# Kernel optimization log

Measured on AMD Instinct MI355X. Metric: run time of the kernel, lower is better.

The kernel has to match this reference:

```python
import jax, jax.numpy as jnp
import numpy as np

B, N, F_IN, H = 16, 1024, 64, 256
NEG = -9e15
ALPHA = 0.2  # LeakyReLU slope


def _leaky(x):
    return jnp.where(x >= 0, x, ALPHA * x)


def setup_inputs() -> dict:
    key = jax.random.key(0)
    ks = jax.random.split(key, 12)
    s = lambda k, shape, fan: jax.random.normal(k, shape, jnp.float32) / np.sqrt(fan)
    node_features = jax.random.normal(ks[0], (B, N, F_IN), jnp.float32)
    adj_matrix = jax.random.randint(ks[1], (B, N, N), 0, 2).astype(jnp.float32)
    return {
        "node_features": node_features,
        "adj_matrix": adj_matrix,
        "emb_W": s(ks[2], (F_IN, H), F_IN),
        "emb_b": jnp.zeros((H,), jnp.float32),
        "W0": s(ks[3], (H, H), H),
        "a1_0": s(ks[4], (H,), H),
        "a2_0": s(ks[5], (H,), H),
        "W1": s(ks[6], (H, H), H),
        "a1_1": s(ks[7], (H,), H),
        "a2_1": s(ks[8], (H,), H),
        "gp_W1": s(ks[9], (H, H), H),
        "gp_b1": jnp.zeros((H,), jnp.float32),
        "gp_W2": s(ks[10], (H, H), H),
        "gp_b2": jnp.zeros((H,), jnp.float32),
    }


def _gat_layer(x, mask, W, a1, a2):
    # x: [B,N,H]; mask: [B,N,N] bool. Equivalent to original concat trick:
    # a([h_i || h_j]) = h_i @ a1 + h_j @ a2 with a.weight split in halves.
    h = jnp.einsum('bnf,fo->bno', x, W)              # [B,N,H]
    s1 = jnp.einsum('bnh,h->bn', h, a1)              # [B,N]
    s2 = jnp.einsum('bnh,h->bn', h, a2)              # [B,N]
    e = _leaky(s1[:, :, None] + s2[:, None, :])      # [B,N,N]
    att = jax.nn.softmax(jnp.where(mask, e, NEG), axis=2)
    # dropout p=0.2 is identity in eval mode
    return jnp.einsum('bij,bjh->bih', att, h)        # [B,N,H]


def reference(node_features, adj_matrix, emb_W, emb_b,
              W0, a1_0, a2_0, W1, a1_1, a2_1,
              gp_W1, gp_b1, gp_W2, gp_b2):
    mask = adj_matrix > 0
    x = jnp.einsum('bnf,fh->bnh', node_features, emb_W) + emb_b
    x = jax.nn.relu(_gat_layer(x, mask, W0, a1_0, a2_0))
    x = jax.nn.relu(_gat_layer(x, mask, W1, a1_1, a2_1))
    g = jnp.mean(x, axis=1) + jnp.max(x, axis=1)     # [B,H]
    g = jax.nn.relu(g @ gp_W1 + gp_b1) @ gp_W2 + gp_b2
    return x, g
```

## Files before the change

### kernel.cpp

```cpp
#include <hip/hip_runtime.h>
#include <hip/hip_bf16.h>

#define B 16
#define N 1024
#define F_IN 64
#define H 256
#define ALPHA 0.2f
#define LOG2E 1.44269504f

typedef __attribute__((ext_vector_type(8))) _Float16 half8;
typedef __attribute__((ext_vector_type(4))) _Float16 half4;
typedef __attribute__((ext_vector_type(4))) float floatx4;
typedef __attribute__((ext_vector_type(16))) float floatx16;

#if __has_builtin(__builtin_amdgcn_exp2f)
#define EXP2F(x) __builtin_amdgcn_exp2f(x)
#else
#define EXP2F(x) exp2f(x)
#endif

__device__ __forceinline__ floatx4 mfma_f16(half8 a, half8 b, floatx4 c) {
    return __builtin_amdgcn_mfma_f32_16x16x32_f16(a, b, c, 0, 0, 0);
}
__device__ __forceinline__ floatx16 mfma32_f16(half8 a, half8 b, floatx16 c) {
    return __builtin_amdgcn_mfma_f32_32x32x16_f16(a, b, c, 0, 0, 0);
}

__global__ __launch_bounds__(256) void k_front(const float* __restrict__ adj,
                                               const float* __restrict__ embW,
                                               const float* __restrict__ W0, const float* __restrict__ W1,
                                               const float* __restrict__ a10, const float* __restrict__ a20,
                                               const float* __restrict__ a11, const float* __restrict__ a21,
                                               unsigned* __restrict__ mask32,
                                               _Float16* __restrict__ wBf,
                                               _Float16* __restrict__ embf,
                                               float* __restrict__ wa1, float* __restrict__ wa2) {
    __shared__ float lds[256 * 17];
    const int blk = blockIdx.x;
    const int t = threadIdx.x;
    const int lane = t & 63;

    if (blk < 1024) {
        const int wv = blk * 4 + (t >> 6);
#pragma unroll 2
        for (int task = wv; task < B * N * 4; task += 4096) {
            const float4 v = *(const float4*)(adj + (size_t)task * 256 + lane * 4);
            unsigned long long b0 = __ballot(v.x > 0.f);
            unsigned long long b1 = __ballot(v.y > 0.f);
            unsigned long long b2 = __ballot(v.z > 0.f);
            unsigned long long b3 = __ballot(v.w > 0.f);
            if (lane < 8) {
                unsigned w0 = (unsigned)((b0 >> (8 * lane)) & 0xff)
                            | ((unsigned)((b1 >> (8 * lane)) & 0xff) << 8)
                            | ((unsigned)((b2 >> (8 * lane)) & 0xff) << 16)
                            | ((unsigned)((b3 >> (8 * lane)) & 0xff) << 24);
                const int jg = task & 3, row = task >> 2;
                mask32[(size_t)row * 32 + jg * 8 + lane] = w0;
            }
        }
        return;
    }
    const int pb = blk - 1024;
    if (pb == 34) {
        for (int s = t; s < 2048; s += 256) {
            const int ln = s & 63, ct2 = s >> 6;
            const int ct = ct2 >> 1, ks2 = ct2 & 1;
            const int q = ln >> 4, lw = ln & 15;
            half8 bf;
#pragma unroll
            for (int e = 0; e < 8; e++)
                bf[e] = (_Float16)embW[(ks2 * 32 + q * 8 + e) * H + ct * 16 + lw];
            *(half8*)(embf + (size_t)s * 8) = bf;
        }
        return;
    }
    if (pb >= 32) {
        const int l = pb - 32;
        const float* W = l ? W1 : W0;
        const float* a1 = l ? a11 : a10;
        const float* a2 = l ? a21 : a20;
        float* a1s = lds;
        float* a2s = lds + 256;
        a1s[t] = a1[t]; a2s[t] = a2[t];
        __syncthreads();
        float v1 = 0.f, v2 = 0.f;
        for (int c = 0; c < H; c += 4) {
            float4 w = *(const float4*)&W[t * H + c];
            v1 += w.x * a1s[c] + w.y * a1s[c + 1] + w.z * a1s[c + 2] + w.w * a1s[c + 3];
            v2 += w.x * a2s[c] + w.y * a2s[c + 1] + w.z * a2s[c + 2] + w.w * a2s[c + 3];
        }
        wa1[l * H + t] = v1;
        wa2[l * H + t] = v2;
        return;
    }
    const int l = pb >> 4, ct = pb & 15;
    const float* W = l ? W1 : W0;
#pragma unroll
    for (int rep = 0; rep < 16; rep++) {
        int idx = rep * 256 + t;
        int k = idx >> 4, cl = idx & 15;
        lds[k * 17 + cl] = W[k * H + ct * 16 + cl];
    }
    __syncthreads();
    const int w = t >> 6;
    const int l15 = lane & 15, quad = lane >> 4;
#pragma unroll
    for (int e = 0; e < 2; e++) {
        const int ks = w * 2 + e;
        half8 bf;
#pragma unroll
        for (int jj = 0; jj < 8; jj++)
            bf[jj] = (_Float16)lds[(ks * 32 + quad * 8 + jj) * 17 + l15];
        *(half8*)(wBf + (size_t)(((l * 16 + ct) * 8 + ks) * 64 + lane) * 8) = bf;
    }
}

#define XS(it, ks) ((((it) * 8 + (ks))) * 520)
template <int EMB>
__global__ __launch_bounds__(256, 4) void k_gemm(const _Float16* __restrict__ xf,
                                                 const float* __restrict__ nf,
                                                 const _Float16* __restrict__ embf,
                                                 const float* __restrict__ embB,
                                                 const _Float16* __restrict__ wBf,
                                                 const float* __restrict__ wa1, const float* __restrict__ wa2,
                                                 _Float16* __restrict__ hB,
                                                 float* __restrict__ s1, float* __restrict__ s2) {
    __shared__ __align__(16) _Float16 sm[8320];
    const int lin = blockIdx.x;
    const int rc = lin >> 1, chalf = lin & 1;
    const int row0 = rc * 32;
    const int t = threadIdx.x;
    const int lane = t & 63, w = t >> 6;
    const int l15 = lane & 15, quad = lane >> 4;

    if (EMB) {
        half8 anf[2][2];
#pragma unroll
        for (int it = 0; it < 2; it++)
#pragma unroll
            for (int ks2 = 0; ks2 < 2; ks2++) {
                const float* src = nf + (size_t)(row0 + it * 16 + l15) * F_IN + ks2 * 32 + quad * 8;
                float4 f0 = *(const float4*)(src);
                float4 f1 = *(const float4*)(src + 4);
                half8 a;
                a[0] = (_Float16)f0.x; a[1] = (_Float16)f0.y;
                a[2] = (_Float16)f0.z; a[3] = (_Float16)f0.w;
                a[4] = (_Float16)f1.x; a[5] = (_Float16)f1.y;
                a[6] = (_Float16)f1.z; a[7] = (_Float16)f1.w;
                anf[it][ks2] = a;
            }
#pragma unroll
        for (int ctl = 0; ctl < 4; ctl++) {
            const int ct = w * 4 + ctl;
            half8 be0 = *(const half8*)(embf + (size_t)((ct * 2 + 0) * 64 + lane) * 8);
            half8 be1 = *(const half8*)(embf + (size_t)((ct * 2 + 1) * 64 + lane) * 8);
            const int col = ct * 16 + l15;
            const float bias = embB[col];
            const int ks = col >> 5, qd = (col >> 3) & 3, e = col & 7;
#pragma unroll
            for (int it = 0; it < 2; it++) {
                floatx4 xa = {0.f, 0.f, 0.f, 0.f};
                xa = mfma_f16(anf[it][0], be0, xa);
                xa = mfma_f16(anf[it][1], be1, xa);
#pragma unroll
                for (int r = 0; r < 4; r++)
                    sm[XS(it, ks) + (qd * 16 + quad * 4 + r) * 8 + e] = (_Float16)(xa[r] + bias);
            }
        }
    } else {
#pragma unroll
        for (int pass = 0; pass < 4; pass++) {
            int idx = pass * 256 + t;
            int row_l = idx >> 5, k8 = idx & 31;
            half8 v = *(const half8*)(xf + (size_t)(row0 + row_l) * H + k8 * 8);
            int it = row_l >> 4, lf = row_l & 15, ks = k8 >> 2, qd = k8 & 3;
            *(half8*)(sm + XS(it, ks) + (qd * 16 + lf) * 8) = v;
        }
    }
    __syncthreads();

    const int ct0 = chalf * 8 + 2 * w;
    const _Float16* pB0 = wBf + (size_t)((ct0 * 8) * 64 + lane) * 8;
    const _Float16* pB1 = wBf + (size_t)(((ct0 + 1) * 8) * 64 + lane) * 8;

    floatx4 acc[2][2];
    floatx4 z = {0.f, 0.f, 0.f, 0.f};
    acc[0][0] = z; acc[0][1] = z; acc[1][0] = z; acc[1][1] = z;
    float sp1a = 0.f, sp2a = 0.f, sp1b = 0.f, sp2b = 0.f;

    half8 B0 = *(const half8*)(pB0);
    half8 B1 = *(const half8*)(pB1);

#pragma unroll
    for (int ks = 0; ks < 8; ks++) {
        half8 nB0 = B0, nB1 = B1;
        if (ks < 7) {
            const int o = (ks + 1) * 512;
            nB0 = *(const half8*)(pB0 + o);
            nB1 = *(const half8*)(pB1 + o);
        }
        half8 A0 = *(const half8*)(sm + XS(0, ks) + lane * 8);
        half8 A1 = *(const half8*)(sm + XS(1, ks) + lane * 8);
        acc[0][0] = mfma_f16(A0, B0, acc[0][0]);
        acc[0][1] = mfma_f16(A0, B1, acc[0][1]);
        acc[1][0] = mfma_f16(A1, B0, acc[1][0]);
        acc[1][1] = mfma_f16(A1, B1, acc[1][1]);
        if (chalf == 0 && w == 0) {
            float4 w1a = *(const float4*)(wa1 + ks * 32 + quad * 8);
            float4 w1b = *(const float4*)(wa1 + ks * 32 + quad * 8 + 4);
            float4 w2a = *(const float4*)(wa2 + ks * 32 + quad * 8);
            float4 w2b = *(const float4*)(wa2 + ks * 32 + quad * 8 + 4);
            float wv1[8] = {w1a.x, w1a.y, w1a.z, w1a.w, w1b.x, w1b.y, w1b.z, w1b.w};
            float wv2[8] = {w2a.x, w2a.y, w2a.z, w2a.w, w2b.x, w2b.y, w2b.z, w2b.w};
#pragma unroll
            for (int j = 0; j < 8; j++) {
                float xa = (float)A0[j];
                float xb = (float)A1[j];
                sp1a += xa * wv1[j]; sp2a += xa * wv2[j];
                sp1b += xb * wv1[j]; sp2b += xb * wv2[j];
            }
        }
        B0 = nB0; B1 = nB1;
    }

    __syncthreads();
    _Float16* trc = sm;
#pragma unroll
    for (int rg = 0; rg < 2; rg++) {
#pragma unroll
        for (int n2 = 0; n2 < 2; n2++) {
            const int c_l = (2 * w + n2) * 16 + l15;
            half4 hv;
            hv[0] = (_Float16)acc[rg][n2][0];
            hv[1] = (_Float16)acc[rg][n2][1];
            hv[2] = (_Float16)acc[rg][n2][2];
            hv[3] = (_Float16)acc[rg][n2][3];
            *(half4*)(trc + c_l * 40 + rg * 16 + quad * 4) = hv;
        }
    }
    __syncthreads();
    {
        const int bb = row0 >> 10, jtb = (row0 >> 5) & 31;
#pragma unroll
        for (int rep = 0; rep < 2; rep++) {
            int slot = rep * 256 + t;
            int l = slot & 63, frag = slot >> 6;
            int k4 = frag >> 1, ks = frag & 1;
            int c_l = k4 * 32 + (l & 31);
            int roff = ks * 16 + (l >> 5) * 8;
            half8 hv = *(const half8*)(trc + c_l * 40 + roff);
            _Float16* dst = hB + ((size_t)((bb * 8 + chalf * 4 + k4) * 32 + jtb) * 2 + ks) * 512 + l * 8;
            *(half8*)dst = hv;
        }
    }
    if (chalf == 0 && w == 0) {
        sp1a += __shfl_xor(sp1a, 16); sp1a += __shfl_xor(sp1a, 32);
        sp2a += __shfl_xor(sp2a, 16); sp2a += __shfl_xor(sp2a, 32);
        sp1b += __shfl_xor(sp1b, 16); sp1b += __shfl_xor(sp1b, 32);
        sp2b += __shfl_xor(sp2b, 16); sp2b += __shfl_xor(sp2b, 32);
        if (quad == 0) {
            s1[row0 + l15] = sp1a; s2[row0 + l15] = sp2a;
            s1[row0 + 16 + l15] = sp1b; s2[row0 + 16 + l15] = sp2b;
        }
    }
}

template <int LAST>
__global__ __launch_bounds__(256, 1) void k_gat(const _Float16* __restrict__ hB,
                                                const float* __restrict__ s1g,
                                                const float* __restrict__ s2g,
                                                const unsigned* __restrict__ mask32,
                                                float* __restrict__ outf,
                                                _Float16* __restrict__ oxf,
                                                float* __restrict__ psum, float* __restrict__ pmax) {
    __shared__ float s2s[N];
    __shared__ unsigned msk[128][33];
    __shared__ float wmax[4];
    __shared__ float red1[4][128];
    __shared__ float red2[4][128];
    const int lin = blockIdx.x;
    const int xcd = lin & 7, sl = lin >> 3;
    const int b = xcd * 2 + (sl & 1);
    const int chunk = (sl >> 1) & 7;
    const int chalf = sl >> 4;
    const int i0 = chunk * 128;
    const int t = threadIdx.x;
    const int lane = t & 63, w = t >> 6;
    const int l31 = lane & 31, hi = lane >> 5;
    const int hi2 = hi * 2, hi8 = hi * 8;

    float tm = -INFINITY;
    for (int idx = t; idx < N; idx += 256) {
        float v = s2g[b * N + idx] * LOG2E;
        s2s[idx] = v;
        tm = fmaxf(tm, v);
    }
#pragma unroll
    for (int off = 1; off <= 32; off <<= 1) tm = fmaxf(tm, __shfl_xor(tm, off));
    if (lane == 0) wmax[w] = tm;
#pragma unroll
    for (int pass = 0; pass < 16; pass++) {
        int idx = pass * 256 + t;
        int r = idx >> 5, wd = idx & 31;
        msk[r][wd] = mask32[(size_t)(b * N + i0 + r) * 32 + wd];
    }
    __syncthreads();
    const float s2maxL = fmaxf(fmaxf(wmax[0], wmax[1]), fmaxf(wmax[2], wmax[3]));

    const float s1L = s1g[b * N + i0 + w * 32 + l31] * LOG2E;
    const float tmx = s1L + s2maxL;
    const float mL = fmaxf(tmx, ALPHA * tmx);
    const float a1c = s1L - mL;
    const float a2c = fmaf(ALPHA, s1L, -mL);

    const _Float16* pb[4][2];
#pragma unroll
    for (int k4 = 0; k4 < 4; k4++)
#pragma unroll
        for (int ks = 0; ks < 2; ks++)
            pb[k4][ks] = hB + ((size_t)(b * 8 + chalf * 4 + k4) * 64 + ks) * 512 + lane * 8;

    floatx16 acc[4];
    floatx16 accl;
#pragma unroll
    for (int r = 0; r < 16; r++) accl[r] = 0.f;
#pragma unroll
    for (int k4 = 0; k4 < 4; k4++) acc[k4] = accl;

    half8 ones;
#pragma unroll
    for (int jj = 0; jj < 8; jj++) ones[jj] = (_Float16)1.0f;

    const float* svp = s2s + hi8;
    const unsigned* mr = &msk[w * 32 + l31][0];

    half8 bufA[4][2], bufB[4][2];
#pragma unroll
    for (int k4 = 0; k4 < 4; k4++) {
        bufA[k4][0] = *(const half8*)(pb[k4][0]);
        bufA[k4][1] = *(const half8*)(pb[k4][1]);
    }

#define GAT_STEP(JT, BUF)                                                      \
    do {                                                                       \
        const unsigned m = mr[JT];                                             \
        float4 sa0 = *(const float4*)(svp + (JT) * 32);                        \
        float4 sb0 = *(const float4*)(svp + (JT) * 32 + 4);                    \
        float4 sa1 = *(const float4*)(svp + (JT) * 32 + 16);                   \
        float4 sb1 = *(const float4*)(svp + (JT) * 32 + 20);                   \
        float sv0[8] = {sa0.x, sa0.y, sa0.z, sa0.w, sb0.x, sb0.y, sb0.z, sb0.w};\
        float sv1[8] = {sa1.x, sa1.y, sa1.z, sa1.w, sb1.x, sb1.y, sb1.z, sb1.w};\
        unsigned mq0 = m >> hi2;                                               \
        unsigned mq1 = m >> (4 + hi2);                                         \
        union { _Float16 h[8]; half8 v; } pk0, pk1;                            \
        _Pragma("unroll")                                                      \
        for (int e = 0; e < 8; e++) {                                          \
            const int bp = (e & 3) * 8 + (e >> 2);                             \
            float u0 = a1c + sv0[e];                                           \
            float v0 = fmaf(ALPHA, sv0[e], a2c);                               \
            float w0 = fmaxf(u0, v0);                                          \
            w0 = ((mq0 >> bp) & 1u) ? w0 : -126.f;                             \
            pk0.h[e] = (_Float16)EXP2F(w0);                                    \
            float u1 = a1c + sv1[e];                                           \
            float v1 = fmaf(ALPHA, sv1[e], a2c);                               \
            float w1 = fmaxf(u1, v1);                                          \
            w1 = ((mq1 >> bp) & 1u) ? w1 : -126.f;                             \
            pk1.h[e] = (_Float16)EXP2F(w1);                                    \
        }                                                                      \
        accl = mfma32_f16(pk0.v, ones, accl);                                  \
        _Pragma("unroll")                                                      \
        for (int k4 = 0; k4 < 4; k4++) acc[k4] = mfma32_f16(pk0.v, BUF[k4][0], acc[k4]); \
        accl = mfma32_f16(pk1.v, ones, accl);                                  \
        _Pragma("unroll")                                                      \
        for (int k4 = 0; k4 < 4; k4++) acc[k4] = mfma32_f16(pk1.v, BUF[k4][1], acc[k4]); \
    } while (0)

    for (int jt = 0; jt < 32; jt += 2) {
        {
            const int o = (jt + 1) * 1024;
#pragma unroll
            for (int k4 = 0; k4 < 4; k4++) {
                bufB[k4][0] = *(const half8*)(pb[k4][0] + o);
                bufB[k4][1] = *(const half8*)(pb[k4][1] + o);
            }
        }
        GAT_STEP(jt, bufA);
        if (jt + 2 < 32) {
            const int o = (jt + 2) * 1024;
#pragma unroll
            for (int k4 = 0; k4 < 4; k4++) {
                bufA[k4][0] = *(const half8*)(pb[k4][0] + o);
                bufA[k4][1] = *(const half8*)(pb[k4][1] + o);
            }
        }
        GAT_STEP(jt + 1, bufB);
    }
#undef GAT_STEP

    float invv[16];
#pragma unroll
    for (int r = 0; r < 16; r++) invv[r] = 1.f / accl[r];

    const size_t rowb = (size_t)b * N + i0 + w * 32 + 4 * hi;
    const int colbase = chalf * 128;
#pragma unroll
    for (int k4 = 0; k4 < 4; k4++) {
        const int c = colbase + k4 * 32 + l31;
        float cs = 0.f, cm = -INFINITY;
#pragma unroll
        for (int reg = 0; reg < 16; reg++) {
            const int roff = (reg & 3) + 8 * (reg >> 2);
            float v = fmaxf(acc[k4][reg] * invv[reg], 0.f);
            if (LAST) {
                outf[(rowb + roff) * H + c] = v;
                cs += v; cm = fmaxf(cm, v);
            } else {
                oxf[(rowb + roff) * H + c] = (_Float16)v;
            }
        }
        if (LAST) {
            cs += __shfl_xor(cs, 32);
            cm = fmaxf(cm, __shfl_xor(cm, 32));
            if (hi == 0) { red1[w][k4 * 32 + l31] = cs; red2[w][k4 * 32 + l31] = cm; }
        }
    }
    if (LAST) {
        __syncthreads();
        if (t < 128) {
            float s = red1[0][t] + red1[1][t] + red1[2][t] + red1[3][t];
            float m = fmaxf(fmaxf(red2[0][t], red2[1][t]), fmaxf(red2[2][t], red2[3][t]));
            psum[(b * 8 + chunk) * H + chalf * 128 + t] = s;
            pmax[(b * 8 + chunk) * H + chalf * 128 + t] = m;
        }
    }
}

__global__ __launch_bounds__(256) void k_pool2(const float* __restrict__ psum,
                                               const float* __restrict__ pmax,
                                               const float* __restrict__ W1, const float* __restrict__ b1,
                                               const float* __restrict__ W2, const float* __restrict__ b2,
                                               float* __restrict__ gout) {
    __shared__ float g_s[H];
    __shared__ float t_s[H];
    const int b = blockIdx.x;
    const int c = threadIdx.x;
    float s = 0.f, m = -INFINITY;
#pragma unroll
    for (int ch = 0; ch < 8; ch++) {
        s += psum[(b * 8 + ch) * H + c];
        m = fmaxf(m, pmax[(b * 8 + ch) * H + c]);
    }
    g_s[c] = s * (1.f / N) + m;
    __syncthreads();
    float a = b1[c];
#pragma unroll 16
    for (int k = 0; k < H; k++) a += g_s[k] * W1[k * H + c];
    t_s[c] = fmaxf(a, 0.f);
    __syncthreads();
    float o = b2[c];
#pragma unroll 16
    for (int k = 0; k < H; k++) o += t_s[k] * W2[k * H + c];
    gout[b * H + c] = o;
}

extern "C" void kernel_launch(void* const* d_in, const int* in_sizes, int n_in,
                              void* d_out, int out_size, void* d_ws, size_t ws_size,
                              hipStream_t stream) {
    const float* nf    = (const float*)d_in[0];
    const float* adj   = (const float*)d_in[1];
    const float* emb_W = (const float*)d_in[2];
    const float* emb_b = (const float*)d_in[3];
    const float* W0    = (const float*)d_in[4];
    const float* a1_0  = (const float*)d_in[5];
    const float* a2_0  = (const float*)d_in[6];
    const float* W1    = (const float*)d_in[7];
    const float* a1_1  = (const float*)d_in[8];
    const float* a2_1  = (const float*)d_in[9];
    const float* gpW1  = (const float*)d_in[10];
    const float* gpb1  = (const float*)d_in[11];
    const float* gpW2  = (const float*)d_in[12];
    const float* gpb2  = (const float*)d_in[13];

    float* xout = (float*)d_out;
    float* gout = xout + B * N * H;

    char* w = (char*)d_ws;
    _Float16* xf     = (_Float16*)(w);
    _Float16* hB     = (_Float16*)(w + 8388608);
    unsigned* mask32 = (unsigned*)(w + 16777216);
    float* s1        = (float*)(w + 18874368);
    float* s2        = (float*)(w + 18939904);
    _Float16* wBf    = (_Float16*)(w + 19005440);
    float* wa1       = (float*)(w + 19267584);
    float* wa2       = (float*)(w + 19269632);
    float* psum      = (float*)(w + 19271680);
    float* pmax      = (float*)(w + 19533824);
    _Float16* embf   = (_Float16*)(w + 19795968);

    k_front<<<1059, 256, 0, stream>>>(adj, emb_W, W0, W1,
                                      a1_0, a2_0, a1_1, a2_1,
                                      mask32, wBf, embf, wa1, wa2);

    k_gemm<1><<<1024, 256, 0, stream>>>(nullptr, nf, embf, emb_b,
                                        wBf, wa1, wa2, hB, s1, s2);
    k_gat<0><<<256, 256, 0, stream>>>(hB, s1, s2, mask32, nullptr, xf,
                                      nullptr, nullptr);

    k_gemm<0><<<1024, 256, 0, stream>>>(xf, nullptr, nullptr, nullptr,
                                        wBf + 65536, wa1 + H, wa2 + H, hB, s1, s2);
    k_gat<1><<<256, 256, 0, stream>>>(hB, s1, s2, mask32, xout, nullptr,
                                      psum, pmax);

    k_pool2<<<B, 256, 0, stream>>>(psum, pmax, gpW1, gpb1, gpW2, gpb2, gout);
}
```

Before: 219.0 us.

## Overlap adjacency bitmask packing with embedding GEMM and fuse pooling into last GAT

The small weight-prep work moves into its own tiny kernel. The adjacency-to-bitmask packing now shares one launch with the first embedding/projection GEMM through interleaved block roles, so the memory-bound mask pass overlaps with the compute-bound GEMM. The graph pooling MLP is folded into the last GAT kernel using a per-batch atomic counter, where the last block to finish does the readout, which removes a separate launch. This adds atomic and ordering complexity, and the counter must be reset each call, which the prep kernel does.

```diff
diff --git a/kernel.cpp b/kernel.cpp
--- a/kernel.cpp
+++ b/kernel.cpp
@@ -26,22 +26,92 @@
     return __builtin_amdgcn_mfma_f32_32x32x16_f16(a, b, c, 0, 0, 0);
 }
 
-__global__ __launch_bounds__(256) void k_front(const float* __restrict__ adj,
-                                               const float* __restrict__ embW,
-                                               const float* __restrict__ W0, const float* __restrict__ W1,
-                                               const float* __restrict__ a10, const float* __restrict__ a20,
-                                               const float* __restrict__ a11, const float* __restrict__ a21,
-                                               unsigned* __restrict__ mask32,
-                                               _Float16* __restrict__ wBf,
-                                               _Float16* __restrict__ embf,
-                                               float* __restrict__ wa1, float* __restrict__ wa2) {
+__global__ __launch_bounds__(256) void k_prep(const float* __restrict__ embW,
+                                              const float* __restrict__ W0, const float* __restrict__ W1,
+                                              const float* __restrict__ a10, const float* __restrict__ a20,
+                                              const float* __restrict__ a11, const float* __restrict__ a21,
+                                              _Float16* __restrict__ wBf,
+                                              _Float16* __restrict__ embf,
+                                              float* __restrict__ wa1, float* __restrict__ wa2,
+                                              int* __restrict__ cnt) {
     __shared__ float lds[256 * 17];
     const int blk = blockIdx.x;
     const int t = threadIdx.x;
     const int lane = t & 63;
 
-    if (blk < 1024) {
-        const int wv = blk * 4 + (t >> 6);
+    if (blk == 34) {
+        if (t < B) cnt[t] = 0;
+        for (int s = t; s < 2048; s += 256) {
+            const int ln = s & 63, ct2 = s >> 6;
+            const int ct = ct2 >> 1, ks2 = ct2 & 1;
+            const int q = ln >> 4, lw = ln & 15;
+            half8 bf;
+#pragma unroll
+            for (int e = 0; e < 8; e++)
+                bf[e] = (_Float16)embW[(ks2 * 32 + q * 8 + e) * H + ct * 16 + lw];
+            *(half8*)(embf + (size_t)s * 8) = bf;
+        }
+        return;
+    }
+    if (blk >= 32) {
+        const int l = blk - 32;
+        const float* W = l ? W1 : W0;
+        const float* a1 = l ? a11 : a10;
+        const float* a2 = l ? a21 : a20;
+        float* a1s = lds;
+        float* a2s = lds + 256;
+        a1s[t] = a1[t]; a2s[t] = a2[t];
+        __syncthreads();
+        float v1 = 0.f, v2 = 0.f;
+        for (int c = 0; c < H; c += 4) {
+            float4 w = *(const float4*)&W[t * H + c];
+            v1 += w.x * a1s[c] + w.y * a1s[c + 1] + w.z * a1s[c + 2] + w.w * a1s[c + 3];
+            v2 += w.x * a2s[c] + w.y * a2s[c + 1] + w.z * a2s[c + 2] + w.w * a2s[c + 3];
+        }
+        wa1[l * H + t] = v1;
+        wa2[l * H + t] = v2;
+        return;
+    }
+    const int l = blk >> 4, ct = blk & 15;
+    const float* W = l ? W1 : W0;
+#pragma unroll
+    for (int rep = 0; rep < 16; rep++) {
+        int idx = rep * 256 + t;
+        int k = idx >> 4, cl = idx & 15;
+        lds[k * 17 + cl] = W[k * H + ct * 16 + cl];
+    }
+    __syncthreads();
+    const int w = t >> 6;
+    const int l15 = lane & 15, quad = lane >> 4;
+#pragma unroll
+    for (int e = 0; e < 2; e++) {
+        const int ks = w * 2 + e;
+        half8 bf;
+#pragma unroll
+        for (int jj = 0; jj < 8; jj++)
+            bf[jj] = (_Float16)lds[(ks * 32 + quad * 8 + jj) * 17 + l15];
+        *(half8*)(wBf + (size_t)(((l * 16 + ct) * 8 + ks) * 64 + lane) * 8) = bf;
+    }
+}
+
+#define XS(it, ks) ((((it) * 8 + (ks))) * 520)
+__global__ __launch_bounds__(256, 4) void k_mix(const float* __restrict__ adj,
+                                                const float* __restrict__ nf,
+                                                const _Float16* __restrict__ embf,
+                                                const float* __restrict__ embB,
+                                                const _Float16* __restrict__ wBf,
+                                                const float* __restrict__ wa1, const float* __restrict__ wa2,
+                                                unsigned* __restrict__ mask32,
+                                                _Float16* __restrict__ hB,
+                                                float* __restrict__ s1, float* __restrict__ s2) {
+    __shared__ __align__(16) _Float16 sm[8320];
+    const int blk = blockIdx.x;
+    const int t = threadIdx.x;
+    const int lane = t & 63;
+
+    if (blk & 1) {
+        const int id = blk >> 1;
+        const int wv = id * 4 + (t >> 6);
 #pragma unroll 2
         for (int task = wv; task < B * N * 4; task += 4096) {
             const float4 v = *(const float4*)(adj + (size_t)task * 256 + lane * 4);
@@ -60,80 +130,14 @@
         }
         return;
     }
-    const int pb = blk - 1024;
-    if (pb == 34) {
-        for (int s = t; s < 2048; s += 256) {
-            const int ln = s & 63, ct2 = s >> 6;
-            const int ct = ct2 >> 1, ks2 = ct2 & 1;
-            const int q = ln >> 4, lw = ln & 15;
-            half8 bf;
-#pragma unroll
-            for (int e = 0; e < 8; e++)
-                bf[e] = (_Float16)embW[(ks2 * 32 + q * 8 + e) * H + ct * 16 + lw];
-            *(half8*)(embf + (size_t)s * 8) = bf;
-        }
-        return;
-    }
-    if (pb >= 32) {
-        const int l = pb - 32;
-        const float* W = l ? W1 : W0;
-        const float* a1 = l ? a11 : a10;
-        const float* a2 = l ? a21 : a20;
-        float* a1s = lds;
-        float* a2s = lds + 256;
-        a1s[t] = a1[t]; a2s[t] = a2[t];
-        __syncthreads();
-        float v1 = 0.f, v2 = 0.f;
-        for (int c = 0; c < H; c += 4) {
-            float4 w = *(const float4*)&W[t * H + c];
-            v1 += w.x * a1s[c] + w.y * a1s[c + 1] + w.z * a1s[c + 2] + w.w * a1s[c + 3];
-            v2 += w.x * a2s[c] + w.y * a2s[c + 1] + w.z * a2s[c + 2] + w.w * a2s[c + 3];
-        }
-        wa1[l * H + t] = v1;
-        wa2[l * H + t] = v2;
-        return;
-    }
-    const int l = pb >> 4, ct = pb & 15;
-    const float* W = l ? W1 : W0;
-#pragma unroll
-    for (int rep = 0; rep < 16; rep++) {
-        int idx = rep * 256 + t;
-        int k = idx >> 4, cl = idx & 15;
-        lds[k * 17 + cl] = W[k * H + ct * 16 + cl];
-    }
-    __syncthreads();
+
+    const int lin = blk >> 1;
+    const int rc = lin >> 1, chalf = lin & 1;
+    const int row0 = rc * 32;
     const int w = t >> 6;
     const int l15 = lane & 15, quad = lane >> 4;
-#pragma unroll
-    for (int e = 0; e < 2; e++) {
-        const int ks = w * 2 + e;
-        half8 bf;
-#pragma unroll
-        for (int jj = 0; jj < 8; jj++)
-            bf[jj] = (_Float16)lds[(ks * 32 + quad * 8 + jj) * 17 + l15];
-        *(half8*)(wBf + (size_t)(((l * 16 + ct) * 8 + ks) * 64 + lane) * 8) = bf;
-    }
-}
-
-#define XS(it, ks) ((((it) * 8 + (ks))) * 520)
-template <int EMB>
-__global__ __launch_bounds__(256, 4) void k_gemm(const _Float16* __restrict__ xf,
-                                                 const float* __restrict__ nf,
-                                                 const _Float16* __restrict__ embf,
-                                                 const float* __restrict__ embB,
-                                                 const _Float16* __restrict__ wBf,
-                                                 const float* __restrict__ wa1, const float* __restrict__ wa2,
-                                                 _Float16* __restrict__ hB,
-                                                 float* __restrict__ s1, float* __restrict__ s2) {
-    __shared__ __align__(16) _Float16 sm[8320];
-    const int lin = blockIdx.x;
-    const int rc = lin >> 1, chalf = lin & 1;
-    const int row0 = rc * 32;
-    const int t = threadIdx.x;
-    const int lane = t & 63, w = t >> 6;
-    const int l15 = lane & 15, quad = lane >> 4;
-
-    if (EMB) {
+
+    {
         half8 anf[2][2];
 #pragma unroll
         for (int it = 0; it < 2; it++)
@@ -166,15 +170,6 @@
                 for (int r = 0; r < 4; r++)
                     sm[XS(it, ks) + (qd * 16 + quad * 4 + r) * 8 + e] = (_Float16)(xa[r] + bias);
             }
-        }
-    } else {
-#pragma unroll
-        for (int pass = 0; pass < 4; pass++) {
-            int idx = pass * 256 + t;
-            int row_l = idx >> 5, k8 = idx & 31;
-            half8 v = *(const half8*)(xf + (size_t)(row0 + row_l) * H + k8 * 8);
-            int it = row_l >> 4, lf = row_l & 15, ks = k8 >> 2, qd = k8 & 3;
-            *(half8*)(sm + XS(it, ks) + (qd * 16 + lf) * 8) = v;
         }
     }
     __syncthreads();
@@ -265,6 +260,115 @@
     }
 }
 
+__global__ __launch_bounds__(256, 4) void k_gemm(const _Float16* __restrict__ xf,
+                                                 const _Float16* __restrict__ wBf,
+                                                 const float* __restrict__ wa1, const float* __restrict__ wa2,
+                                                 _Float16* __restrict__ hB,
+                                                 float* __restrict__ s1, float* __restrict__ s2) {
+    __shared__ __align__(16) _Float16 sm[8320];
+    const int lin = blockIdx.x;
+    const int rc = lin >> 1, chalf = lin & 1;
+    const int row0 = rc * 32;
+    const int t = threadIdx.x;
+    const int lane = t & 63, w = t >> 6;
+    const int l15 = lane & 15, quad = lane >> 4;
+
+#pragma unroll
+    for (int pass = 0; pass < 4; pass++) {
+        int idx = pass * 256 + t;
+        int row_l = idx >> 5, k8 = idx & 31;
+        half8 v = *(const half8*)(xf + (size_t)(row0 + row_l) * H + k8 * 8);
+        int it = row_l >> 4, lf = row_l & 15, ks = k8 >> 2, qd = k8 & 3;
+        *(half8*)(sm + XS(it, ks) + (qd * 16 + lf) * 8) = v;
+    }
+    __syncthreads();
+
+    const int ct0 = chalf * 8 + 2 * w;
+    const _Float16* pB0 = wBf + (size_t)((ct0 * 8) * 64 + lane) * 8;
+    const _Float16* pB1 = wBf + (size_t)(((ct0 + 1) * 8) * 64 + lane) * 8;
+
+    floatx4 acc[2][2];
+    floatx4 z = {0.f, 0.f, 0.f, 0.f};
+    acc[0][0] = z; acc[0][1] = z; acc[1][0] = z; acc[1][1] = z;
+    float sp1a = 0.f, sp2a = 0.f, sp1b = 0.f, sp2b = 0.f;
+
+    half8 B0 = *(const half8*)(pB0);
+    half8 B1 = *(const half8*)(pB1);
+
+#pragma unroll
+    for (int ks = 0; ks < 8; ks++) {
+        half8 nB0 = B0, nB1 = B1;
+        if (ks < 7) {
+            const int o = (ks + 1) * 512;
+            nB0 = *(const half8*)(pB0 + o);
+            nB1 = *(const half8*)(pB1 + o);
+        }
+        half8 A0 = *(const half8*)(sm + XS(0, ks) + lane * 8);
+        half8 A1 = *(const half8*)(sm + XS(1, ks) + lane * 8);
+        acc[0][0] = mfma_f16(A0, B0, acc[0][0]);
+        acc[0][1] = mfma_f16(A0, B1, acc[0][1]);
+        acc[1][0] = mfma_f16(A1, B0, acc[1][0]);
+        acc[1][1] = mfma_f16(A1, B1, acc[1][1]);
+        if (chalf == 0 && w == 0) {
+            float4 w1a = *(const float4*)(wa1 + ks * 32 + quad * 8);
+            float4 w1b = *(const float4*)(wa1 + ks * 32 + quad * 8 + 4);
+            float4 w2a = *(const float4*)(wa2 + ks * 32 + quad * 8);
+            float4 w2b = *(const float4*)(wa2 + ks * 32 + quad * 8 + 4);
+            float wv1[8] = {w1a.x, w1a.y, w1a.z, w1a.w, w1b.x, w1b.y, w1b.z, w1b.w};
+            float wv2[8] = {w2a.x, w2a.y, w2a.z, w2a.w, w2b.x, w2b.y, w2b.z, w2b.w};
+#pragma unroll
+            for (int j = 0; j < 8; j++) {
+                float xa = (float)A0[j];
+                float xb = (float)A1[j];
+                sp1a += xa * wv1[j]; sp2a += xa * wv2[j];
+                sp1b += xb * wv1[j]; sp2b += xb * wv2[j];
+            }
+        }
+        B0 = nB0; B1 = nB1;
+    }
+
+    __syncthreads();
+    _Float16* trc = sm;
+#pragma unroll
+    for (int rg = 0; rg < 2; rg++) {
+#pragma unroll
+        for (int n2 = 0; n2 < 2; n2++) {
+            const int c_l = (2 * w + n2) * 16 + l15;
+            half4 hv;
+            hv[0] = (_Float16)acc[rg][n2][0];
+            hv[1] = (_Float16)acc[rg][n2][1];
+            hv[2] = (_Float16)acc[rg][n2][2];
+            hv[3] = (_Float16)acc[rg][n2][3];
+            *(half4*)(trc + c_l * 40 + rg * 16 + quad * 4) = hv;
+        }
+    }
+    __syncthreads();
+    {
+        const int bb = row0 >> 10, jtb = (row0 >> 5) & 31;
+#pragma unroll
+        for (int rep = 0; rep < 2; rep++) {
+            int slot = rep * 256 + t;
+            int l = slot & 63, frag = slot >> 6;
+            int k4 = frag >> 1, ks = frag & 1;
+            int c_l = k4 * 32 + (l & 31);
+            int roff = ks * 16 + (l >> 5) * 8;
+            half8 hv = *(const half8*)(trc + c_l * 40 + roff);
+            _Float16* dst = hB + ((size_t)((bb * 8 + chalf * 4 + k4) * 32 + jtb) * 2 + ks) * 512 + l * 8;
+            *(half8*)dst = hv;
+        }
+    }
+    if (chalf == 0 && w == 0) {
+        sp1a += __shfl_xor(sp1a, 16); sp1a += __shfl_xor(sp1a, 32);
+        sp2a += __shfl_xor(sp2a, 16); sp2a += __shfl_xor(sp2a, 32);
+        sp1b += __shfl_xor(sp1b, 16); sp1b += __shfl_xor(sp1b, 32);
+        sp2b += __shfl_xor(sp2b, 16); sp2b += __shfl_xor(sp2b, 32);
+        if (quad == 0) {
+            s1[row0 + l15] = sp1a; s2[row0 + l15] = sp2a;
+            s1[row0 + 16 + l15] = sp1b; s2[row0 + 16 + l15] = sp2b;
+        }
+    }
+}
+
 template <int LAST>
 __global__ __launch_bounds__(256, 1) void k_gat(const _Float16* __restrict__ hB,
                                                 const float* __restrict__ s1g,
@@ -272,12 +376,16 @@
                                                 const unsigned* __restrict__ mask32,
                                                 float* __restrict__ outf,
                                                 _Float16* __restrict__ oxf,
-                                                float* __restrict__ psum, float* __restrict__ pmax) {
+                                                float* __restrict__ psum, float* __restrict__ pmax,
+                                                const float* __restrict__ gpW1, const float* __restrict__ gpb1,
+                                                const float* __restrict__ gpW2, const float* __restrict__ gpb2,
+                                                float* __restrict__ gout, int* __restrict__ cnt) {
     __shared__ float s2s[N];
     __shared__ unsigned msk[128][33];
     __shared__ float wmax[4];
     __shared__ float red1[4][128];
     __shared__ float red2[4][128];
+    __shared__ int lastf;
     const int lin = blockIdx.x;
     const int xcd = lin & 7, sl = lin >> 3;
     const int b = xcd * 2 + (sl & 1);
@@ -429,38 +537,43 @@
         if (t < 128) {
             float s = red1[0][t] + red1[1][t] + red1[2][t] + red1[3][t];
             float m = fmaxf(fmaxf(red2[0][t], red2[1][t]), fmaxf(red2[2][t], red2[3][t]));
-            psum[(b * 8 + chunk) * H + chalf * 128 + t] = s;
-            pmax[(b * 8 + chunk) * H + chalf * 128 + t] = m;
-        }
-    }
-}
-
-__global__ __launch_bounds__(256) void k_pool2(const float* __restrict__ psum,
-                                               const float* __restrict__ pmax,
-                                               const float* __restrict__ W1, const float* __restrict__ b1,
-                                               const float* __restrict__ W2, const float* __restrict__ b2,
-                                               float* __restrict__ gout) {
-    __shared__ float g_s[H];
-    __shared__ float t_s[H];
-    const int b = blockIdx.x;
-    const int c = threadIdx.x;
-    float s = 0.f, m = -INFINITY;
-#pragma unroll
-    for (int ch = 0; ch < 8; ch++) {
-        s += psum[(b * 8 + ch) * H + c];
-        m = fmaxf(m, pmax[(b * 8 + ch) * H + c]);
-    }
-    g_s[c] = s * (1.f / N) + m;
-    __syncthreads();
-    float a = b1[c];
+            __hip_atomic_store(&psum[(b * 8 + chunk) * H + chalf * 128 + t], s,
+                               __ATOMIC_RELAXED, __HIP_MEMORY_SCOPE_AGENT);
+            __hip_atomic_store(&pmax[(b * 8 + chunk) * H + chalf * 128 + t], m,
+                               __ATOMIC_RELAXED, __HIP_MEMORY_SCOPE_AGENT);
+        }
+        asm volatile("s_waitcnt vmcnt(0)" ::: "memory");
+        __syncthreads();
+        if (t == 0) {
+            int old = atomicAdd(&cnt[b], 1);
+            lastf = (old == 15) ? 1 : 0;
+        }
+        __syncthreads();
+        if (lastf) {
+            float* g_s = s2s;
+            float* t_s = s2s + 256;
+            const int c = t;
+            float s = 0.f, m = -INFINITY;
+#pragma unroll
+            for (int ch = 0; ch < 8; ch++) {
+                s += __hip_atomic_load(&psum[(b * 8 + ch) * H + c],
+                                       __ATOMIC_RELAXED, __HIP_MEMORY_SCOPE_AGENT);
+                m = fmaxf(m, __hip_atomic_load(&pmax[(b * 8 + ch) * H + c],
+                                               __ATOMIC_RELAXED, __HIP_MEMORY_SCOPE_AGENT));
+            }
+            g_s[c] = s * (1.f / N) + m;
+            __syncthreads();
+            float a = gpb1[c];
 #pragma unroll 16
-    for (int k = 0; k < H; k++) a += g_s[k] * W1[k * H + c];
-    t_s[c] = fmaxf(a, 0.f);
-    __syncthreads();
-    float o = b2[c];
+            for (int k = 0; k < H; k++) a += g_s[k] * gpW1[k * H + c];
+            t_s[c] = fmaxf(a, 0.f);
+            __syncthreads();
+            float o = gpb2[c];
 #pragma unroll 16
-    for (int k = 0; k < H; k++) o += t_s[k] * W2[k * H + c];
-    gout[b * H + c] = o;
+            for (int k = 0; k < H; k++) o += t_s[k] * gpW2[k * H + c];
+            gout[b * H + c] = o;
+        }
+    }
 }
 
 extern "C" void kernel_launch(void* const* d_in, const int* in_sizes, int n_in,
@@ -496,20 +609,19 @@
     float* psum      = (float*)(w + 19271680);
     float* pmax      = (float*)(w + 19533824);
     _Float16* embf   = (_Float16*)(w + 19795968);
-
-    k_front<<<1059, 256, 0, stream>>>(adj, emb_W, W0, W1,
-                                      a1_0, a2_0, a1_1, a2_1,
-                                      mask32, wBf, embf, wa1, wa2);
-
-    k_gemm<1><<<1024, 256, 0, stream>>>(nullptr, nf, embf, emb_b,
-                                        wBf, wa1, wa2, hB, s1, s2);
+    int* cnt         = (int*)(w + 19828736);
+
+    k_prep<<<35, 256, 0, stream>>>(emb_W, W0, W1, a1_0, a2_0, a1_1, a2_1,
+                                   wBf, embf, wa1, wa2, cnt);
+
+    k_mix<<<2048, 256, 0, stream>>>(adj, nf, embf, emb_b, wBf, wa1, wa2,
+                                    mask32, hB, s1, s2);
     k_gat<0><<<256, 256, 0, stream>>>(hB, s1, s2, mask32, nullptr, xf,
-                                      nullptr, nullptr);
-
-    k_gemm<0><<<1024, 256, 0, stream>>>(xf, nullptr, nullptr, nullptr,
-                                        wBf + 65536, wa1 + H, wa2 + H, hB, s1, s2);
+                                      nullptr, nullptr, nullptr, nullptr,
+                                      nullptr, nullptr, nullptr, nullptr);
+
+    k_gemm<<<1024, 256, 0, stream>>>(xf, wBf + 65536, wa1 + H, wa2 + H, hB, s1, s2);
     k_gat<1><<<256, 256, 0, stream>>>(hB, s1, s2, mask32, xout, nullptr,
-                                      psum, pmax);
-
-    k_pool2<<<B, 256, 0, stream>>>(psum, pmax, gpW1, gpb1, gpW2, gpb2, gout);
+                                      psum, pmax, gpW1, gpb1, gpW2, gpb2,
+                                      gout, cnt);
 }
```

Result: no change. 222.9 us (+1.8%).
